# Kernel optimization log

Measured on AMD Instinct MI355X. Metric: run time of the kernel, lower is better.

Reference implementation:

```python
import jax, jax.numpy as jnp
import numpy as np

HIDDEN = 4096
FFN = 14336
GS = 64  # groupsize


def dequant2(qw, scales, zeros, N):
    """Unpack 2-bit HQQ weights. qw: (N//4, K) int32, scales/zeros: (G, K).
    Returns W of shape (N, K) float: (bits - zeros[n % G]) * scales[n % G]."""
    G = scales.shape[0]
    n = jnp.arange(N)
    packed = qw[n // 4]                      # (N, K)
    shift = ((3 - (n % 4)) * 2).astype(qw.dtype)  # per-row bit shift
    vals = (packed >> shift[:, None]) & 3    # (N, K) 2-bit codes
    g = n % G
    return (vals.astype(scales.dtype) - zeros[g]) * scales[g]


def setup_inputs() -> dict:
    key = jax.random.key(0)
    ks = jax.random.split(key, 12)
    x = jax.random.normal(ks[0], (512, HIDDEN), dtype=jnp.float32)
    qw1 = jax.random.randint(ks[1], (FFN // 4, HIDDEN), 0, 256, dtype=jnp.int32)
    qw3 = jax.random.randint(ks[2], (FFN // 4, HIDDEN), 0, 256, dtype=jnp.int32)
    qw2 = jax.random.randint(ks[3], (HIDDEN // 4, FFN), 0, 256, dtype=jnp.int32)
    G1 = FFN // GS
    G2 = HIDDEN // GS
    s1 = jax.random.uniform(ks[4], (G1, HIDDEN), dtype=jnp.float32) * 0.05
    z1 = jax.random.uniform(ks[5], (G1, HIDDEN), dtype=jnp.float32)
    s3 = jax.random.uniform(ks[6], (G1, HIDDEN), dtype=jnp.float32) * 0.05
    z3 = jax.random.uniform(ks[7], (G1, HIDDEN), dtype=jnp.float32)
    s2 = jax.random.uniform(ks[8], (G2, FFN), dtype=jnp.float32) * 0.05
    z2 = jax.random.uniform(ks[9], (G2, FFN), dtype=jnp.float32)
    return {"x": x, "qw1": qw1, "s1": s1, "z1": z1, "qw3": qw3, "s3": s3,
            "z3": z3, "qw2": qw2, "s2": s2, "z2": z2, "groupsize": GS}


def reference(x, qw1, s1, z1, qw3, s3, z3, qw2, s2, z2, groupsize):
    # gate / up projections: C = x @ W^T, W dequantized to (N, K)
    w1 = dequant2(qw1, s1, z1, FFN)      # (FFN, HIDDEN)
    w3 = dequant2(qw3, s3, z3, FFN)      # (FFN, HIDDEN)
    w2 = dequant2(qw2, s2, z2, HIDDEN)   # (HIDDEN, FFN)
    gate = jnp.einsum('mk,nk->mn', x, w1)   # (M, FFN)
    up = jnp.einsum('mk,nk->mn', x, w3)     # (M, FFN)
    h = jax.nn.silu(gate) * up               # SwiGLU
    out = jnp.einsum('mf,hf->mh', h, w2)     # (M, HIDDEN)
    return out
```

## Files before the change

kernel.cpp:

```cpp
#include <hip/hip_runtime.h>
#include <hip/hip_fp16.h>
#include <stdint.h>

#define HIDDEN 4096
#define FFN    14336
#define MDIM   512
#define G1     224
#define G2     64
#define BK     64

typedef _Float16 f16x8 __attribute__((ext_vector_type(8)));
typedef float f32x4 __attribute__((ext_vector_type(4)));

__device__ __forceinline__ void gl_lds16(const void* g, void* l) {
    __builtin_amdgcn_global_load_lds(
        (const __attribute__((address_space(1))) uint32_t*)g,
        (__attribute__((address_space(3))) uint32_t*)l, 16, 0, 0);
}

#define SCHED0() __builtin_amdgcn_sched_barrier(0);
#define LGKM_BAR()                                            \
    asm volatile("s_waitcnt lgkmcnt(0)" ::: "memory");        \
    __builtin_amdgcn_s_barrier();                             \
    __builtin_amdgcn_sched_barrier(0);


__global__ void cvt_x_kernel(const float* __restrict__ x, ushort* __restrict__ xb) {
    int i = blockIdx.x * blockDim.x + threadIdx.x;
    float4 v = ((const float4*)x)[i];
    __half2 a = __floats2half2_rn(v.x, v.y);
    __half2 b = __floats2half2_rn(v.z, v.w);
    ((uint2*)xb)[i] = make_uint2(__builtin_bit_cast(uint32_t, a),
                                 __builtin_bit_cast(uint32_t, b));
}

__global__ void build_sz_kernel(const float* __restrict__ s, const float* __restrict__ z,
                                uint32_t* __restrict__ outp) {
    int i = blockIdx.x * blockDim.x + threadIdx.x;
    float s0 = s[2 * i], s1 = s[2 * i + 1];
    float z0 = z[2 * i], z1 = z[2 * i + 1];
    __half2 hs = __floats2half2_rn(s0, s1);
    __half2 hn = __floats2half2_rn(-z0 * s0, -z1 * s1);
    ((uint2*)outp)[i] = make_uint2(__builtin_bit_cast(uint32_t, hs),
                                   __builtin_bit_cast(uint32_t, hn));
}

__device__ __forceinline__ uint32_t deq2(uint32_t w0, uint32_t w1, uint32_t sh,
                                         uint32_t spair, uint32_t npair) {
    uint32_t c0 = (w0 >> sh) & 3u;
    uint32_t c1 = (w1 >> sh) & 3u;
    uint32_t sel = 0x01000100u + c0 * 0x0202u + c1 * 0x02020000u;
    uint32_t codes = __builtin_amdgcn_perm(0x42004000u, 0x3C000000u, sel);
    __half2 r = __hfma2(__builtin_bit_cast(__half2, codes),
                        __builtin_bit_cast(__half2, spair),
                        __builtin_bit_cast(__half2, npair));
    return __builtin_bit_cast(uint32_t, r);
}


__global__ __launch_bounds__(256, 2)
void gemm_gateup(const ushort* __restrict__ xb, const uint32_t* __restrict__ qw1,
                 const uint32_t* __restrict__ sz1, const uint32_t* __restrict__ qw3,
                 const uint32_t* __restrict__ sz3, ushort* __restrict__ hbuf) {
    __shared__ ushort sAl[2][256 * 64];
    __shared__ ushort sB1[32 * 64];
    __shared__ ushort sB2[32 * 64];

    const int tid = threadIdx.x;
    const int idx = ((blockIdx.x & 7) * 112) + (blockIdx.x >> 3);
    const int mt = idx & 1, nt = idx >> 1;
    const int m0 = mt * 256, n0 = nt * 32;

    const int lane = tid & 63, w = tid >> 6;
    const int wm = w * 64;
    const int frow = lane & 15, fk = (lane >> 4) * 8;
    const int sw = (frow & 7) << 3;

    const int qs = (lane & 7) ^ ((lane >> 3) & 7);
    const ushort* apS[8];
#pragma unroll
    for (int s = 0; s < 8; ++s) {
        int r = s * 32 + w * 8 + (lane >> 3);
        apS[s] = xb + (size_t)(m0 + r) * HIDDEN + qs * 8;
    }

    const int bi = tid & 127;
    const int rp = bi >> 3;
    const int kc = (bi & 7) * 8;
    const int row0 = rp * 2;
    const int g0 = (n0 + row0) % G1;
    const uint32_t* qp = (tid < 128 ? qw1 : qw3) + (size_t)(n0 / 4 + (rp >> 1)) * HIDDEN + kc;
    const uint32_t* zp = (tid < 128 ? sz1 : sz3) + (size_t)g0 * HIDDEN + kc;
    ushort* sB = (tid < 128) ? sB1 : sB2;
    const uint32_t sh0 = 6u - 4u * (uint32_t)(rp & 1);

    f32x4 accG[4][2], accU[4][2];
#pragma unroll
    for (int i = 0; i < 4; ++i)
#pragma unroll
        for (int j = 0; j < 2; ++j) {
            accG[i][j] = (f32x4){0.f, 0.f, 0.f, 0.f};
            accU[i][j] = (f32x4){0.f, 0.f, 0.f, 0.f};
        }

    uint4 pw0, pw1;
    uint4 pz0, pz1, pz2, pz3;
    int cur = 0;

#define GU_GLDA(k0d, curd)                                                     \
    { _Pragma("unroll")                                                        \
      for (int s = 0; s < 8; ++s)                                              \
          gl_lds16(apS[s] + (k0d), &sAl[curd][(s * 256 + w * 64) * 8]); }

#define GU_LD(k0q)                                                             \
    pw0 = *(const uint4*)(qp + (k0q));                                         \
    pw1 = *(const uint4*)(qp + (k0q) + 4);                                     \
    pz0 = *(const uint4*)(zp + (k0q));                                         \
    pz1 = *(const uint4*)(zp + (k0q) + 4);                                     \
    pz2 = *(const uint4*)(zp + HIDDEN + (k0q));                                \
    pz3 = *(const uint4*)(zp + HIDDEN + (k0q) + 4);

#define GU_DEQ()                                                               \
    { const uint32_t wv[8] = {pw0.x, pw0.y, pw0.z, pw0.w,                      \
                              pw1.x, pw1.y, pw1.z, pw1.w};                     \
      {   const uint32_t sp[4] = {pz0.x, pz0.z, pz1.x, pz1.z};                 \
          const uint32_t np[4] = {pz0.y, pz0.w, pz1.y, pz1.w};                 \
          uint32_t o[4];                                                       \
          _Pragma("unroll")                                                    \
          for (int j = 0; j < 4; ++j)                                          \
              o[j] = deq2(wv[2*j], wv[2*j+1], sh0, sp[j], np[j]);              \
          *(uint4*)&sB[row0 * 64 + (kc ^ ((row0 & 7) << 3))] =                 \
              make_uint4(o[0], o[1], o[2], o[3]);                              \
      }                                                                        \
      {   const uint32_t sp[4] = {pz2.x, pz2.z, pz3.x, pz3.z};                 \
          const uint32_t np[4] = {pz2.y, pz2.w, pz3.y, pz3.w};                 \
          uint32_t o[4];                                                       \
          _Pragma("unroll")                                                    \
          for (int j = 0; j < 4; ++j)                                          \
              o[j] = deq2(wv[2*j], wv[2*j+1], sh0 - 2u, sp[j], np[j]);         \
          const int row1 = row0 + 1;                                           \
          *(uint4*)&sB[row1 * 64 + (kc ^ ((row1 & 7) << 3))] =                 \
              make_uint4(o[0], o[1], o[2], o[3]);                              \
      } }

#define GU_COMP()                                                              \
    { _Pragma("unroll")                                                        \
      for (int kk = 0; kk < 2; ++kk) {                                         \
          const int col = ((kk * 32) + fk) ^ sw;                               \
          f16x8 af[4], bg[2], bu[2];                                           \
          _Pragma("unroll")                                                    \
          for (int i = 0; i < 4; ++i)                                          \
              af[i] = *(const f16x8*)&sAl[cur][(wm + i * 16 + frow) * 64 + col]; \
          bg[0] = *(const f16x8*)&sB1[frow * 64 + col];                        \
          bg[1] = *(const f16x8*)&sB1[(16 + frow) * 64 + col];                 \
          bu[0] = *(const f16x8*)&sB2[frow * 64 + col];                        \
          bu[1] = *(const f16x8*)&sB2[(16 + frow) * 64 + col];                 \
          _Pragma("unroll")                                                    \
          for (int mi = 0; mi < 4; ++mi)                                       \
              _Pragma("unroll")                                                \
              for (int ni = 0; ni < 2; ++ni) {                                 \
                  accG[mi][ni] = __builtin_amdgcn_mfma_f32_16x16x32_f16(af[mi], bg[ni], accG[mi][ni], 0, 0, 0); \
                  accU[mi][ni] = __builtin_amdgcn_mfma_f32_16x16x32_f16(af[mi], bu[ni], accU[mi][ni], 0, 0, 0); \
              } } }

    GU_GLDA(0, 0)
    GU_LD(0)
    asm volatile("s_waitcnt vmcnt(0)" ::: "memory"); SCHED0()
    GU_DEQ()
    GU_LD(BK)
    LGKM_BAR()

    for (int t = 0; t < 62; ++t) {
        const int k0 = t * BK;
        GU_GLDA(k0 + BK, cur ^ 1) SCHED0()
        GU_COMP()
        LGKM_BAR()
        GU_DEQ()
        SCHED0()
        GU_LD(k0 + 2 * BK)
        SCHED0()
        asm volatile("s_waitcnt vmcnt(6)" ::: "memory"); SCHED0()
        LGKM_BAR()
        cur ^= 1;
    }
    GU_GLDA(63 * BK, cur ^ 1) SCHED0()
    GU_COMP()
    LGKM_BAR()
    GU_DEQ()
    SCHED0()
    asm volatile("s_waitcnt vmcnt(0)" ::: "memory"); SCHED0()
    LGKM_BAR()
    cur ^= 1;
    GU_COMP()

    ushort* so = &sAl[0][0];
    const int rb = (lane >> 4) * 4, cb = lane & 15;
#pragma unroll
    for (int mi = 0; mi < 4; ++mi)
#pragma unroll
        for (int ni = 0; ni < 2; ++ni) {
            f32x4 g = accG[mi][ni], u = accU[mi][ni];
            const int row = wm + mi * 16 + rb;
            const int colx = ni * 16 + cb;
#pragma unroll
            for (int r = 0; r < 4; ++r) {
                float gv = g[r];
                float hv = __fdividef(gv, 1.0f + __expf(-gv)) * u[r];
                __half hh = __float2half(hv);
                so[(row + r) * 32 + colx] = __builtin_bit_cast(ushort, hh);
            }
        }
    __syncthreads();
    {
        ushort* dst = hbuf + (size_t)(m0 + tid) * FFN + n0;
        const ushort* src = so + tid * 32;
#pragma unroll
        for (int i = 0; i < 4; ++i)
            *(uint4*)(dst + 8 * i) = *(const uint4*)(src + 8 * i);
    }
#undef GU_GLDA
#undef GU_LD
#undef GU_DEQ
#undef GU_COMP
}


__global__ __launch_bounds__(256, 2)
void gemm_down(const ushort* __restrict__ hb, const uint32_t* __restrict__ qw2,
               const uint32_t* __restrict__ sz2, float* __restrict__ part) {
    __shared__ ushort sAl[2][256 * 64];
    __shared__ ushort sBd[32 * 64];

    const int tid = threadIdx.x;
    const int idx = ((blockIdx.x & 7) * 64) + (blockIdx.x >> 3);
    const int mt = idx & 1, nt = (idx >> 1) & 127, sk = idx >> 8;
    const int m0 = mt * 256, n0 = nt * 32;
    const int kbeg = sk * (FFN / 2);

    const int lane = tid & 63, w = tid >> 6;
    const int wm = w * 64;
    const int frow = lane & 15, fk = (lane >> 4) * 8;
    const int sw = (frow & 7) << 3;

    const int qs = (lane & 7) ^ ((lane >> 3) & 7);
    const ushort* apS[8];
#pragma unroll
    for (int s = 0; s < 8; ++s) {
        int r = s * 32 + w * 8 + (lane >> 3);
        apS[s] = hb + (size_t)(m0 + r) * FFN + kbeg + qs * 8;
    }

    const int r = tid >> 3;
    const int kc = (tid & 7) * 8;
    const int g = ((nt & 1) * 32) + r;
    const uint32_t* qp = qw2 + (size_t)(n0 / 4 + (r >> 2)) * FFN + kbeg + kc;
    const uint32_t* zp = sz2 + (size_t)g * FFN + kbeg + kc;
    const uint32_t sh = 6u - 2u * (uint32_t)(r & 3);

    f32x4 acc[4][2];
#pragma unroll
    for (int i = 0; i < 4; ++i)
#pragma unroll
        for (int j = 0; j < 2; ++j) acc[i][j] = (f32x4){0.f, 0.f, 0.f, 0.f};

    uint4 pw0, pw1;
    uint4 pz0, pz1;
    int cur = 0;

#define GD_GLDA(k0d, curd)                                                     \
    { _Pragma("unroll")                                                        \
      for (int s = 0; s < 8; ++s)                                              \
          gl_lds16(apS[s] + (k0d), &sAl[curd][(s * 256 + w * 64) * 8]); }

#define GD_LD(k0q)                                                             \
    pw0 = *(const uint4*)(qp + (k0q));                                         \
    pw1 = *(const uint4*)(qp + (k0q) + 4);                                     \
    pz0 = *(const uint4*)(zp + (k0q));                                         \
    pz1 = *(const uint4*)(zp + (k0q) + 4);

#define GD_DEQ()                                                               \
    { const uint32_t wv[8] = {pw0.x, pw0.y, pw0.z, pw0.w,                      \
                              pw1.x, pw1.y, pw1.z, pw1.w};                     \
      const uint32_t sp[4] = {pz0.x, pz0.z, pz1.x, pz1.z};                     \
      const uint32_t np[4] = {pz0.y, pz0.w, pz1.y, pz1.w};                     \
      uint32_t o[4];                                                           \
      _Pragma("unroll")                                                        \
      for (int j = 0; j < 4; ++j)                                              \
          o[j] = deq2(wv[2*j], wv[2*j+1], sh, sp[j], np[j]);                   \
      *(uint4*)&sBd[r * 64 + (kc ^ ((r & 7) << 3))] =                          \
          make_uint4(o[0], o[1], o[2], o[3]); }

#define GD_COMP()                                                              \
    { _Pragma("unroll")                                                        \
      for (int kk = 0; kk < 2; ++kk) {                                         \
          const int col = ((kk * 32) + fk) ^ sw;                               \
          f16x8 af[4], bf[2];                                                  \
          _Pragma("unroll")                                                    \
          for (int i = 0; i < 4; ++i)                                          \
              af[i] = *(const f16x8*)&sAl[cur][(wm + i * 16 + frow) * 64 + col]; \
          bf[0] = *(const f16x8*)&sBd[frow * 64 + col];                        \
          bf[1] = *(const f16x8*)&sBd[(16 + frow) * 64 + col];                 \
          _Pragma("unroll")                                                    \
          for (int mi = 0; mi < 4; ++mi)                                       \
              _Pragma("unroll")                                                \
              for (int ni = 0; ni < 2; ++ni)                                   \
                  acc[mi][ni] = __builtin_amdgcn_mfma_f32_16x16x32_f16(af[mi], bf[ni], acc[mi][ni], 0, 0, 0); \
      } }

    GD_GLDA(0, 0)
    GD_LD(0)
    asm volatile("s_waitcnt vmcnt(0)" ::: "memory"); SCHED0()
    GD_DEQ()
    GD_LD(BK)
    LGKM_BAR()

    for (int t = 0; t < 110; ++t) {
        const int k0 = t * BK;
        GD_GLDA(k0 + BK, cur ^ 1) SCHED0()
        GD_COMP()
        LGKM_BAR()
        GD_DEQ()
        SCHED0()
        GD_LD(k0 + 2 * BK)
        SCHED0()
        asm volatile("s_waitcnt vmcnt(4)" ::: "memory"); SCHED0()
        LGKM_BAR()
        cur ^= 1;
    }
    GD_GLDA(111 * BK, cur ^ 1) SCHED0()
    GD_COMP()
    LGKM_BAR()
    GD_DEQ()
    SCHED0()
    asm volatile("s_waitcnt vmcnt(0)" ::: "memory"); SCHED0()
    LGKM_BAR()
    cur ^= 1;
    GD_COMP()

    float* pp = part + (size_t)sk * MDIM * HIDDEN;
    const int rb = (lane >> 4) * 4, cb = lane & 15;
#pragma unroll
    for (int mi = 0; mi < 4; ++mi)
#pragma unroll
        for (int ni = 0; ni < 2; ++ni) {
            f32x4 a = acc[mi][ni];
            const int mm = m0 + wm + mi * 16 + rb;
            const int nn = n0 + ni * 16 + cb;
#pragma unroll
            for (int rr = 0; rr < 4; ++rr) pp[(size_t)(mm + rr) * HIDDEN + nn] = a[rr];
        }
#undef GD_GLDA
#undef GD_LD
#undef GD_DEQ
#undef GD_COMP
}


__global__ void reduce_out(const float* __restrict__ part, float* __restrict__ out) {
    int i = blockIdx.x * blockDim.x + threadIdx.x;
    const int Q = MDIM * HIDDEN / 4;
    float4 a = ((const float4*)part)[i];
    float4 b = ((const float4*)part)[i + Q];
    float4 o;
    o.x = a.x + b.x; o.y = a.y + b.y; o.z = a.z + b.z; o.w = a.w + b.w;
    ((float4*)out)[i] = o;
}


extern "C" void kernel_launch(void* const* d_in, const int* in_sizes, int n_in,
                              void* d_out, int out_size, void* d_ws, size_t ws_size,
                              hipStream_t stream) {
    (void)in_sizes; (void)n_in; (void)out_size; (void)ws_size;

    const float* x  = (const float*)d_in[0];
    const uint32_t* qw1 = (const uint32_t*)d_in[1];
    const float* s1 = (const float*)d_in[2];
    const float* z1 = (const float*)d_in[3];
    const uint32_t* qw3 = (const uint32_t*)d_in[4];
    const float* s3 = (const float*)d_in[5];
    const float* z3 = (const float*)d_in[6];
    const uint32_t* qw2 = (const uint32_t*)d_in[7];
    const float* s2 = (const float*)d_in[8];
    const float* z2 = (const float*)d_in[9];
    float* out = (float*)d_out;

    char* ws = (char*)d_ws;
    ushort*   xb   = (ushort*)ws;
    uint32_t* szp1 = (uint32_t*)(ws + (size_t)MDIM * HIDDEN * 2);
    uint32_t* szp3 = szp1 + (size_t)G1 * HIDDEN;
    uint32_t* szp2 = szp3 + (size_t)G1 * HIDDEN;
    ushort*   hbuf = (ushort*)(szp2 + (size_t)G2 * FFN);
    float*    part = (float*)((char*)hbuf + (size_t)MDIM * FFN * 2);

    cvt_x_kernel<<<(MDIM * HIDDEN / 4) / 256, 256, 0, stream>>>(x, xb);
    build_sz_kernel<<<(G1 * HIDDEN / 2) / 256, 256, 0, stream>>>(s1, z1, szp1);
    build_sz_kernel<<<(G1 * HIDDEN / 2) / 256, 256, 0, stream>>>(s3, z3, szp3);
    build_sz_kernel<<<(G2 * FFN / 2) / 256, 256, 0, stream>>>(s2, z2, szp2);

    gemm_gateup<<<(FFN / 32) * (MDIM / 256), 256, 0, stream>>>(xb, qw1, szp1, qw3, szp3, hbuf);
    gemm_down<<<2 * (MDIM / 256) * (HIDDEN / 32), 256, 0, stream>>>(hbuf, qw2, szp2, part);
    reduce_out<<<(MDIM * HIDDEN / 4) / 256, 256, 0, stream>>>(part, out);
}
```

Measured before the change: 350.2 us.

## Double-buffer dequantized B tiles and use one barrier per K step

```diff
diff --git a/kernel.cpp b/kernel.cpp
--- a/kernel.cpp
+++ b/kernel.cpp
@@ -19,10 +19,6 @@
 }
 
 #define SCHED0() __builtin_amdgcn_sched_barrier(0);
-#define LGKM_BAR()                                            \
-    asm volatile("s_waitcnt lgkmcnt(0)" ::: "memory");        \
-    __builtin_amdgcn_s_barrier();                             \
-    __builtin_amdgcn_sched_barrier(0);
 
 
 __global__ void cvt_x_kernel(const float* __restrict__ x, ushort* __restrict__ xb) {
@@ -63,8 +59,8 @@
                  const uint32_t* __restrict__ sz1, const uint32_t* __restrict__ qw3,
                  const uint32_t* __restrict__ sz3, ushort* __restrict__ hbuf) {
     __shared__ ushort sAl[2][256 * 64];
-    __shared__ ushort sB1[32 * 64];
-    __shared__ ushort sB2[32 * 64];
+    __shared__ ushort sB1[2][32 * 64];
+    __shared__ ushort sB2[2][32 * 64];
 
     const int tid = threadIdx.x;
     const int idx = ((blockIdx.x & 7) * 112) + (blockIdx.x >> 3);
@@ -91,7 +87,7 @@
     const int g0 = (n0 + row0) % G1;
     const uint32_t* qp = (tid < 128 ? qw1 : qw3) + (size_t)(n0 / 4 + (rp >> 1)) * HIDDEN + kc;
     const uint32_t* zp = (tid < 128 ? sz1 : sz3) + (size_t)g0 * HIDDEN + kc;
-    ushort* sB = (tid < 128) ? sB1 : sB2;
+    ushort (*sB)[32 * 64] = (tid < 128) ? sB1 : sB2;
     const uint32_t sh0 = 6u - 4u * (uint32_t)(rp & 1);
 
     f32x4 accG[4][2], accU[4][2];
@@ -103,58 +99,57 @@
             accU[i][j] = (f32x4){0.f, 0.f, 0.f, 0.f};
         }
 
-    uint4 pw0, pw1;
-    uint4 pz0, pz1, pz2, pz3;
-    int cur = 0;
-
-#define GU_GLDA(k0d, curd)                                                     \
+    uint4 pwA0, pwA1, pzA0, pzA1, pzA2, pzA3;
+    uint4 pwB0, pwB1, pzB0, pzB1, pzB2, pzB3;
+
+#define GU_GLDA(k0d, wbuf)                                                     \
     { _Pragma("unroll")                                                        \
       for (int s = 0; s < 8; ++s)                                              \
-          gl_lds16(apS[s] + (k0d), &sAl[curd][(s * 256 + w * 64) * 8]); }
-
-#define GU_LD(k0q)                                                             \
-    pw0 = *(const uint4*)(qp + (k0q));                                         \
-    pw1 = *(const uint4*)(qp + (k0q) + 4);                                     \
-    pz0 = *(const uint4*)(zp + (k0q));                                         \
-    pz1 = *(const uint4*)(zp + (k0q) + 4);                                     \
-    pz2 = *(const uint4*)(zp + HIDDEN + (k0q));                                \
-    pz3 = *(const uint4*)(zp + HIDDEN + (k0q) + 4);
-
-#define GU_DEQ()                                                               \
-    { const uint32_t wv[8] = {pw0.x, pw0.y, pw0.z, pw0.w,                      \
-                              pw1.x, pw1.y, pw1.z, pw1.w};                     \
-      {   const uint32_t sp[4] = {pz0.x, pz0.z, pz1.x, pz1.z};                 \
-          const uint32_t np[4] = {pz0.y, pz0.w, pz1.y, pz1.w};                 \
+          gl_lds16(apS[s] + (k0d), &sAl[wbuf][(s * 256 + w * 64) * 8]); }
+
+#define GU_LD(PW0, PW1, PZ0, PZ1, PZ2, PZ3, k0q)                               \
+    PW0 = *(const uint4*)(qp + (k0q));                                         \
+    PW1 = *(const uint4*)(qp + (k0q) + 4);                                     \
+    PZ0 = *(const uint4*)(zp + (k0q));                                         \
+    PZ1 = *(const uint4*)(zp + (k0q) + 4);                                     \
+    PZ2 = *(const uint4*)(zp + HIDDEN + (k0q));                                \
+    PZ3 = *(const uint4*)(zp + HIDDEN + (k0q) + 4);
+
+#define GU_DEQ(wbuf, PW0, PW1, PZ0, PZ1, PZ2, PZ3)                             \
+    { const uint32_t wv[8] = {(PW0).x, (PW0).y, (PW0).z, (PW0).w,              \
+                              (PW1).x, (PW1).y, (PW1).z, (PW1).w};             \
+      {   const uint32_t sp[4] = {(PZ0).x, (PZ0).z, (PZ1).x, (PZ1).z};         \
+          const uint32_t np[4] = {(PZ0).y, (PZ0).w, (PZ1).y, (PZ1).w};         \
           uint32_t o[4];                                                       \
           _Pragma("unroll")                                                    \
           for (int j = 0; j < 4; ++j)                                          \
               o[j] = deq2(wv[2*j], wv[2*j+1], sh0, sp[j], np[j]);              \
-          *(uint4*)&sB[row0 * 64 + (kc ^ ((row0 & 7) << 3))] =                 \
+          *(uint4*)&sB[wbuf][row0 * 64 + (kc ^ ((row0 & 7) << 3))] =           \
               make_uint4(o[0], o[1], o[2], o[3]);                              \
       }                                                                        \
-      {   const uint32_t sp[4] = {pz2.x, pz2.z, pz3.x, pz3.z};                 \
-          const uint32_t np[4] = {pz2.y, pz2.w, pz3.y, pz3.w};                 \
+      {   const uint32_t sp[4] = {(PZ2).x, (PZ2).z, (PZ3).x, (PZ3).z};         \
+          const uint32_t np[4] = {(PZ2).y, (PZ2).w, (PZ3).y, (PZ3).w};         \
           uint32_t o[4];                                                       \
           _Pragma("unroll")                                                    \
           for (int j = 0; j < 4; ++j)                                          \
               o[j] = deq2(wv[2*j], wv[2*j+1], sh0 - 2u, sp[j], np[j]);         \
           const int row1 = row0 + 1;                                           \
-          *(uint4*)&sB[row1 * 64 + (kc ^ ((row1 & 7) << 3))] =                 \
+          *(uint4*)&sB[wbuf][row1 * 64 + (kc ^ ((row1 & 7) << 3))] =           \
               make_uint4(o[0], o[1], o[2], o[3]);                              \
       } }
 
-#define GU_COMP()                                                              \
+#define GU_COMP(rbuf)                                                          \
     { _Pragma("unroll")                                                        \
       for (int kk = 0; kk < 2; ++kk) {                                         \
           const int col = ((kk * 32) + fk) ^ sw;                               \
           f16x8 af[4], bg[2], bu[2];                                           \
           _Pragma("unroll")                                                    \
           for (int i = 0; i < 4; ++i)                                          \
-              af[i] = *(const f16x8*)&sAl[cur][(wm + i * 16 + frow) * 64 + col]; \
-          bg[0] = *(const f16x8*)&sB1[frow * 64 + col];                        \
-          bg[1] = *(const f16x8*)&sB1[(16 + frow) * 64 + col];                 \
-          bu[0] = *(const f16x8*)&sB2[frow * 64 + col];                        \
-          bu[1] = *(const f16x8*)&sB2[(16 + frow) * 64 + col];                 \
+              af[i] = *(const f16x8*)&sAl[rbuf][(wm + i * 16 + frow) * 64 + col]; \
+          bg[0] = *(const f16x8*)&sB1[rbuf][frow * 64 + col];                  \
+          bg[1] = *(const f16x8*)&sB1[rbuf][(16 + frow) * 64 + col];           \
+          bu[0] = *(const f16x8*)&sB2[rbuf][frow * 64 + col];                  \
+          bu[1] = *(const f16x8*)&sB2[rbuf][(16 + frow) * 64 + col];           \
           _Pragma("unroll")                                                    \
           for (int mi = 0; mi < 4; ++mi)                                       \
               _Pragma("unroll")                                                \
@@ -163,35 +158,33 @@
                   accU[mi][ni] = __builtin_amdgcn_mfma_f32_16x16x32_f16(af[mi], bu[ni], accU[mi][ni], 0, 0, 0); \
               } } }
 
+#define GU_STEP(k0s, WBUF, RBUF, PW0, PW1, PZ0, PZ1, PZ2, PZ3, DOPF, VMS)      \
+    { GU_GLDA((k0s) + BK, WBUF) SCHED0()                                       \
+      GU_DEQ(WBUF, PW0, PW1, PZ0, PZ1, PZ2, PZ3)                               \
+      if (DOPF) { GU_LD(PW0, PW1, PZ0, PZ1, PZ2, PZ3, (k0s) + 3 * BK) }        \
+      GU_COMP(RBUF)                                                            \
+      asm volatile("s_waitcnt vmcnt(" VMS ") lgkmcnt(0)" ::: "memory");        \
+      __builtin_amdgcn_s_barrier();                                            \
+      SCHED0() }
+
     GU_GLDA(0, 0)
-    GU_LD(0)
+    GU_LD(pwA0, pwA1, pzA0, pzA1, pzA2, pzA3, 0)
     asm volatile("s_waitcnt vmcnt(0)" ::: "memory"); SCHED0()
-    GU_DEQ()
-    GU_LD(BK)
-    LGKM_BAR()
-
-    for (int t = 0; t < 62; ++t) {
-        const int k0 = t * BK;
-        GU_GLDA(k0 + BK, cur ^ 1) SCHED0()
-        GU_COMP()
-        LGKM_BAR()
-        GU_DEQ()
-        SCHED0()
-        GU_LD(k0 + 2 * BK)
-        SCHED0()
-        asm volatile("s_waitcnt vmcnt(6)" ::: "memory"); SCHED0()
-        LGKM_BAR()
-        cur ^= 1;
-    }
-    GU_GLDA(63 * BK, cur ^ 1) SCHED0()
-    GU_COMP()
-    LGKM_BAR()
-    GU_DEQ()
+    GU_DEQ(0, pwA0, pwA1, pzA0, pzA1, pzA2, pzA3)
+    GU_LD(pwA0, pwA1, pzA0, pzA1, pzA2, pzA3, BK)
+    GU_LD(pwB0, pwB1, pzB0, pzB1, pzB2, pzB3, 2 * BK)
+    asm volatile("s_waitcnt lgkmcnt(0)" ::: "memory");
+    __builtin_amdgcn_s_barrier();
     SCHED0()
-    asm volatile("s_waitcnt vmcnt(0)" ::: "memory"); SCHED0()
-    LGKM_BAR()
-    cur ^= 1;
-    GU_COMP()
+
+    for (int t = 0; t < 60; t += 2) {
+        GU_STEP(t * BK,       1, 0, pwA0, pwA1, pzA0, pzA1, pzA2, pzA3, 1, "6")
+        GU_STEP((t + 1) * BK, 0, 1, pwB0, pwB1, pzB0, pzB1, pzB2, pzB3, 1, "6")
+    }
+    GU_STEP(60 * BK, 1, 0, pwA0, pwA1, pzA0, pzA1, pzA2, pzA3, 1, "6")
+    GU_STEP(61 * BK, 0, 1, pwB0, pwB1, pzB0, pzB1, pzB2, pzB3, 0, "0")
+    GU_STEP(62 * BK, 1, 0, pwA0, pwA1, pzA0, pzA1, pzA2, pzA3, 0, "0")
+    GU_COMP(1)
 
     ushort* so = &sAl[0][0];
     const int rb = (lane >> 4) * 4, cb = lane & 15;
@@ -222,6 +215,7 @@
 #undef GU_LD
 #undef GU_DEQ
 #undef GU_COMP
+#undef GU_STEP
 }
 
 
@@ -229,7 +223,7 @@
 void gemm_down(const ushort* __restrict__ hb, const uint32_t* __restrict__ qw2,
                const uint32_t* __restrict__ sz2, float* __restrict__ part) {
     __shared__ ushort sAl[2][256 * 64];
-    __shared__ ushort sBd[32 * 64];
+    __shared__ ushort sBd[2][32 * 64];
 
     const int tid = threadIdx.x;
     const int idx = ((blockIdx.x & 7) * 64) + (blockIdx.x >> 3);
@@ -263,43 +257,42 @@
 #pragma unroll
         for (int j = 0; j < 2; ++j) acc[i][j] = (f32x4){0.f, 0.f, 0.f, 0.f};
 
-    uint4 pw0, pw1;
-    uint4 pz0, pz1;
-    int cur = 0;
-
-#define GD_GLDA(k0d, curd)                                                     \
+    uint4 pwA0, pwA1, pzA0, pzA1;
+    uint4 pwB0, pwB1, pzB0, pzB1;
+
+#define GD_GLDA(k0d, wbuf)                                                     \
     { _Pragma("unroll")                                                        \
       for (int s = 0; s < 8; ++s)                                              \
-          gl_lds16(apS[s] + (k0d), &sAl[curd][(s * 256 + w * 64) * 8]); }
-
-#define GD_LD(k0q)                                                             \
-    pw0 = *(const uint4*)(qp + (k0q));                                         \
-    pw1 = *(const uint4*)(qp + (k0q) + 4);                                     \
-    pz0 = *(const uint4*)(zp + (k0q));                                         \
-    pz1 = *(const uint4*)(zp + (k0q) + 4);
-
-#define GD_DEQ()                                                               \
-    { const uint32_t wv[8] = {pw0.x, pw0.y, pw0.z, pw0.w,                      \
-                              pw1.x, pw1.y, pw1.z, pw1.w};                     \
-      const uint32_t sp[4] = {pz0.x, pz0.z, pz1.x, pz1.z};                     \
-      const uint32_t np[4] = {pz0.y, pz0.w, pz1.y, pz1.w};                     \
+          gl_lds16(apS[s] + (k0d), &sAl[wbuf][(s * 256 + w * 64) * 8]); }
+
+#define GD_LD(PW0, PW1, PZ0, PZ1, k0q)                                         \
+    PW0 = *(const uint4*)(qp + (k0q));                                         \
+    PW1 = *(const uint4*)(qp + (k0q) + 4);                                     \
+    PZ0 = *(const uint4*)(zp + (k0q));                                         \
+    PZ1 = *(const uint4*)(zp + (k0q) + 4);
+
+#define GD_DEQ(wbuf, PW0, PW1, PZ0, PZ1)                                       \
+    { const uint32_t wv[8] = {(PW0).x, (PW0).y, (PW0).z, (PW0).w,              \
+                              (PW1).x, (PW1).y, (PW1).z, (PW1).w};             \
+      const uint32_t sp[4] = {(PZ0).x, (PZ0).z, (PZ1).x, (PZ1).z};             \
+      const uint32_t np[4] = {(PZ0).y, (PZ0).w, (PZ1).y, (PZ1).w};             \
       uint32_t o[4];                                                           \
       _Pragma("unroll")                                                        \
       for (int j = 0; j < 4; ++j)                                              \
           o[j] = deq2(wv[2*j], wv[2*j+1], sh, sp[j], np[j]);                   \
-      *(uint4*)&sBd[r * 64 + (kc ^ ((r & 7) << 3))] =                          \
+      *(uint4*)&sBd[wbuf][r * 64 + (kc ^ ((r & 7) << 3))] =                    \
           make_uint4(o[0], o[1], o[2], o[3]); }
 
-#define GD_COMP()                                                              \
+#define GD_COMP(rbuf)                                                          \
     { _Pragma("unroll")                                                        \
       for (int kk = 0; kk < 2; ++kk) {                                         \
           const int col = ((kk * 32) + fk) ^ sw;                               \
           f16x8 af[4], bf[2];                                                  \
           _Pragma("unroll")                                                    \
           for (int i = 0; i < 4; ++i)                                          \
-              af[i] = *(const f16x8*)&sAl[cur][(wm + i * 16 + frow) * 64 + col]; \
-          bf[0] = *(const f16x8*)&sBd[frow * 64 + col];                        \
-          bf[1] = *(const f16x8*)&sBd[(16 + frow) * 64 + col];                 \
+              af[i] = *(const f16x8*)&sAl[rbuf][(wm + i * 16 + frow) * 64 + col]; \
+          bf[0] = *(const f16x8*)&sBd[rbuf][frow * 64 + col];                  \
+          bf[1] = *(const f16x8*)&sBd[rbuf][(16 + frow) * 64 + col];           \
           _Pragma("unroll")                                                    \
           for (int mi = 0; mi < 4; ++mi)                                       \
               _Pragma("unroll")                                                \
@@ -307,35 +300,33 @@
                   acc[mi][ni] = __builtin_amdgcn_mfma_f32_16x16x32_f16(af[mi], bf[ni], acc[mi][ni], 0, 0, 0); \
       } }
 
+#define GD_STEP(k0s, WBUF, RBUF, PW0, PW1, PZ0, PZ1, DOPF, VMS)                \
+    { GD_GLDA((k0s) + BK, WBUF) SCHED0()                                       \
+      GD_DEQ(WBUF, PW0, PW1, PZ0, PZ1)                                         \
+      if (DOPF) { GD_LD(PW0, PW1, PZ0, PZ1, (k0s) + 3 * BK) }                  \
+      GD_COMP(RBUF)                                                            \
+      asm volatile("s_waitcnt vmcnt(" VMS ") lgkmcnt(0)" ::: "memory");        \
+      __builtin_amdgcn_s_barrier();                                            \
+      SCHED0() }
+
     GD_GLDA(0, 0)
-    GD_LD(0)
+    GD_LD(pwA0, pwA1, pzA0, pzA1, 0)
     asm volatile("s_waitcnt vmcnt(0)" ::: "memory"); SCHED0()
-    GD_DEQ()
-    GD_LD(BK)
-    LGKM_BAR()
-
-    for (int t = 0; t < 110; ++t) {
-        const int k0 = t * BK;
-        GD_GLDA(k0 + BK, cur ^ 1) SCHED0()
-        GD_COMP()
-        LGKM_BAR()
-        GD_DEQ()
-        SCHED0()
-        GD_LD(k0 + 2 * BK)
-        SCHED0()
-        asm volatile("s_waitcnt vmcnt(4)" ::: "memory"); SCHED0()
-        LGKM_BAR()
-        cur ^= 1;
-    }
-    GD_GLDA(111 * BK, cur ^ 1) SCHED0()
-    GD_COMP()
-    LGKM_BAR()
-    GD_DEQ()
+    GD_DEQ(0, pwA0, pwA1, pzA0, pzA1)
+    GD_LD(pwA0, pwA1, pzA0, pzA1, BK)
+    GD_LD(pwB0, pwB1, pzB0, pzB1, 2 * BK)
+    asm volatile("s_waitcnt lgkmcnt(0)" ::: "memory");
+    __builtin_amdgcn_s_barrier();
     SCHED0()
-    asm volatile("s_waitcnt vmcnt(0)" ::: "memory"); SCHED0()
-    LGKM_BAR()
-    cur ^= 1;
-    GD_COMP()
+
+    for (int t = 0; t < 108; t += 2) {
+        GD_STEP(t * BK,       1, 0, pwA0, pwA1, pzA0, pzA1, 1, "4")
+        GD_STEP((t + 1) * BK, 0, 1, pwB0, pwB1, pzB0, pzB1, 1, "4")
+    }
+    GD_STEP(108 * BK, 1, 0, pwA0, pwA1, pzA0, pzA1, 1, "4")
+    GD_STEP(109 * BK, 0, 1, pwB0, pwB1, pzB0, pzB1, 0, "0")
+    GD_STEP(110 * BK, 1, 0, pwA0, pwA1, pzA0, pzA1, 0, "0")
+    GD_COMP(1)
 
     float* pp = part + (size_t)sk * MDIM * HIDDEN;
     const int rb = (lane >> 4) * 4, cb = lane & 15;
@@ -353,6 +344,7 @@
 #undef GD_LD
 #undef GD_DEQ
 #undef GD_COMP
+#undef GD_STEP
 }
 
 
```

Measured after the change: 335.4 us. 1.04x faster.
